# Performance work log

Measured on AMD Instinct MI355X. Metric: run time of the kernel, lower is better.

The kernel has to match this reference:

```python
import jax, jax.numpy as jnp
import numpy as np

B, T, N, DIN, U, K, C = 32, 256, 128, 16, 64, 2, 4
M = K + 1  # num diffusion matrices per support (I, P, 2P^2-I, ...)


def setup_inputs() -> dict:
    key = jax.random.key(0)
    ks = jax.random.split(key, 10)
    w = lambda k, shape: jax.random.normal(k, shape, jnp.float32) * 0.05
    inp = {}
    inp["input_seq"] = jax.random.normal(ks[0], (B, T, N, DIN), jnp.float32)
    inp["seq_lengths"] = jax.random.randint(ks[1], (B,), 1, T + 1)
    # scaled dense support (graph laplacian surrogate) for numerical stability
    inp["support"] = jax.random.normal(ks[2], (N, N), jnp.float32) / N
    inp["W0_gate"] = w(ks[3], ((DIN + U) * M, 2 * U))
    inp["b0_gate"] = jnp.ones((2 * U,), jnp.float32)  # bias_start=1.0
    inp["W0_cand"] = w(ks[4], ((DIN + U) * M, U))
    inp["b0_cand"] = jnp.zeros((U,), jnp.float32)
    inp["W1_gate"] = w(ks[5], (2 * U * M, 2 * U))
    inp["b1_gate"] = jnp.ones((2 * U,), jnp.float32)
    inp["W1_cand"] = w(ks[6], (2 * U * M, U))
    inp["b1_cand"] = jnp.zeros((U,), jnp.float32)
    inp["W_fc"] = w(ks[7], (U, C))
    inp["b_fc"] = jnp.zeros((C,), jnp.float32)
    return inp


def _gconv(x, support, W, b):
    # x: (B, N, Cin). Chebyshev-style diffusion: [x, Px, 2P(Px)-x, ...]
    x0 = x
    x1 = jnp.einsum('mn,bnc->bmc', support, x0)
    xs = [x0, x1]
    for _ in range(2, K + 1):
        x2 = 2.0 * jnp.einsum('mn,bnc->bmc', support, x1) - x0
        xs.append(x2)
        x0, x1 = x1, x2
    # stack on last axis -> (B, N, Cin, M) -> (B, N, Cin*M), matching the
    # torch reshape order (input feature major, matrix minor)
    xc = jnp.stack(xs, axis=-1).reshape(x.shape[0], x.shape[1], -1)
    return xc @ W + b


def _cell(x, h, support, Wg, bg, Wc, bc):
    # x: (B,N,Din), h: (B,N,U)
    val = jax.nn.sigmoid(_gconv(jnp.concatenate([x, h], axis=-1), support, Wg, bg))
    r, u = jnp.split(val, 2, axis=-1)
    c = jnp.tanh(_gconv(jnp.concatenate([x, r * h], axis=-1), support, Wc, bc))
    return u * h + (1.0 - u) * c


def _run_layer(x_seq, support, Wg, bg, Wc, bc):
    # x_seq: (T, B, N, D)
    def step(h, x):
        h2 = _cell(x, h, support, Wg, bg, Wc, bc)
        return h2, h2
    h0 = jnp.zeros((x_seq.shape[1], N, U), x_seq.dtype)
    _, out = jax.lax.scan(step, h0, x_seq)
    return out  # (T, B, N, U)


def reference(input_seq, seq_lengths, support, W0_gate, b0_gate, W0_cand, b0_cand,
              W1_gate, b1_gate, W1_cand, b1_cand, W_fc, b_fc):
    x = jnp.transpose(input_seq, (1, 0, 2, 3))  # (T,B,N,DIN)
    h1 = _run_layer(x, support, W0_gate, b0_gate, W0_cand, b0_cand)
    h2 = _run_layer(h1, support, W1_gate, b1_gate, W1_cand, b1_cand)
    out_seq = jnp.transpose(h2, (1, 0, 2, 3))  # (B,T,N,U)
    idx = seq_lengths - 1  # last relevant timestep per sequence
    last = out_seq[jnp.arange(out_seq.shape[0]), idx]  # (B,N,U)
    # dropout is identity in eval mode
    logits = jax.nn.relu(last) @ W_fc + b_fc  # (B,N,C)
    return jnp.max(logits, axis=1)  # max-pool over nodes -> (B,C)
```

## Files before the change

kernel.cpp:

```cpp
#include <hip/hip_runtime.h>

#define B_   32
#define T_   256
#define N_   128
#define DIN_ 16
#define U_   64

#define PD 456
#define PT 136
#define LDS_BYTES ((N_*PD + N_*PT)*2)

#define WT0G_OFF 0
#define WT0C_OFF (128*256)
#define WT1G_OFF (WT0C_OFF + 64*256)
#define WT1C_OFF (WT1G_OFF + 128*384)
#define WT_TOTAL (WT1C_OFF + 64*384)
#define S2_OFF   WT_TOTAL
#define FIFO_OFF (S2_OFF + 128*128)
#define FIFO_SLOT(bb,tt) (FIFO_OFF + ((bb)*8 + ((tt)&7))*8192)
#define FLG_BYTE ((FIFO_OFF + 32*8*8192)*2)
#define FLG_USH  4096
#define FIFO2_OFF (FIFO_OFF + 32*8*8192 + FLG_USH)
#define FIFO2_SLOT(bb,tt) (FIFO2_OFF + ((bb)*4 + ((tt)&3))*16384)

typedef __attribute__((ext_vector_type(8))) short bfrag;
typedef __attribute__((ext_vector_type(4))) float ffrag;
typedef __attribute__((ext_vector_type(4))) unsigned short us4;
typedef __attribute__((ext_vector_type(2))) unsigned short us2;
typedef unsigned long long ull;

#define SYNC() asm volatile("s_waitcnt lgkmcnt(0)\n\ts_barrier" ::: "memory")
#define MFMA16(a,b,c) __builtin_amdgcn_mfma_f32_16x16x32_bf16(a,b,c,0,0,0)

__device__ __forceinline__ unsigned short f2b(float x) {
  union { float f; unsigned u; } v; v.f = x;
  return (unsigned short)((v.u + 0x7fffu + ((v.u >> 16) & 1u)) >> 16);
}
__device__ __forceinline__ float sigm(float x) {
  float e = __expf(-x);
  return __builtin_amdgcn_rcpf(1.f + e);
}
__device__ __forceinline__ float tanh_(float x) {
  float e = __expf(2.f * x);
  return 1.f - 2.f * __builtin_amdgcn_rcpf(1.f + e);
}

__device__ __forceinline__ float wval0(const float* w, int ncol, int co, int k) {
  if (k < 16)  return w[(k*3+0)*ncol+co] - w[(k*3+2)*ncol+co];
  if (k < 48)  { int j=k-16, c=j>>1;
                 return (j&1) ? 2.f*w[(c*3+2)*ncol+co] : w[(c*3+1)*ncol+co]; }
  if (k < 64)  return 0.f;
  if (k < 128) { int c=16+(k-64); return w[(c*3+0)*ncol+co] - w[(c*3+2)*ncol+co]; }
  { int j=k-128, c=16+(j>>1);
    return (j&1) ? 2.f*w[(c*3+2)*ncol+co] : w[(c*3+1)*ncol+co]; }
}
__device__ __forceinline__ float wval1(const float* w, int ncol, int co, int k) {
  if (k < 64)  return w[(k*3+0)*ncol+co] - w[(k*3+2)*ncol+co];
  if (k < 192) { int j=k-64, c=j>>1;
                 return (j&1) ? 2.f*w[(c*3+2)*ncol+co] : w[(c*3+1)*ncol+co]; }
  if (k < 256) { int c=64+(k-192); return w[(c*3+0)*ncol+co] - w[(c*3+2)*ncol+co]; }
  { int j=k-256, c=64+(j>>1);
    return (j&1) ? 2.f*w[(c*3+2)*ncol+co] : w[(c*3+1)*ncol+co]; }
}
__device__ __forceinline__ float wval0c(const float* w, int ncol, int co, int k) {
  if (k < 64)  return wval0(w, ncol, co, k);
  if (k < 192) return wval0(w, ncol, co, k + 64);
  return wval0(w, ncol, co, k - 128);
}
__device__ __forceinline__ float wval1c(const float* w, int ncol, int co, int k) {
  if (k < 192) return wval1(w, ncol, co, k);
  if (k < 320) return wval1(w, ncol, co, k + 64);
  return wval1(w, ncol, co, k - 128);
}

__global__ void setup_wt(const float* __restrict__ w0g, const float* __restrict__ w0c,
                         const float* __restrict__ w1g, const float* __restrict__ w1c,
                         unsigned short* __restrict__ wt) {
  int i = blockIdx.x * blockDim.x + threadIdx.x;
  if (i >= WT_TOTAL) return;
  float v;
  if (i < WT0C_OFF)      { int co = i >> 8, k = i & 255;                 v = wval0 (w0g, 128, co, k); }
  else if (i < WT1G_OFF) { int j = i - WT0C_OFF; v = wval0c(w0c, 64, j >> 8, j & 255); }
  else if (i < WT1C_OFF) { int j = i - WT1G_OFF; v = wval1 (w1g, 128, j / 384, j % 384); }
  else                   { int j = i - WT1C_OFF; v = wval1c(w1c, 64, j / 384, j % 384); }
  wt[i] = f2b(v);
}

__global__ void setup_s2(const float* __restrict__ sup, unsigned short* __restrict__ s2) {
  int idx = blockIdx.x * blockDim.x + threadIdx.x;
  int i = idx >> 7, j = idx & 127;
  float acc = 0.f;
#pragma unroll 4
  for (int k = 0; k < 128; ++k) acc += sup[i*128 + k] * sup[k*128 + j];
  s2[idx] = f2b(acc);
}

__global__ void zero_flags(unsigned short* __restrict__ wt) {
  int* flg = (int*)((char*)wt + FLG_BYTE);
  for (int i = threadIdx.x; i < 2048; i += blockDim.x) flg[i] = 0;
}

template<int KT>
__device__ __forceinline__ void gateR(ffrag (&acc)[4][2],
    const bfrag (&bwr)[KT], const bfrag (&bwu)[KT],
    const unsigned short* __restrict__ arowB, const int lq) {
#pragma unroll
  for (int ks = 0; ks < KT; ++ks) {
    bfrag a[4];
#pragma unroll
    for (int i = 0; i < 4; ++i)
      a[i] = *(const bfrag*)&arowB[16*i*PD + 32*ks + 8*lq];
#pragma unroll
    for (int i = 0; i < 4; ++i) {
      acc[i][0] = MFMA16(a[i], bwr[ks], acc[i][0]);
      acc[i][1] = MFMA16(a[i], bwu[ks], acc[i][1]);
    }
  }
}
template<int KT>
__device__ __forceinline__ void candR(ffrag (&acc)[4], bfrag (&bw)[4],
    const unsigned short* __restrict__ arowB, const int (&kofs)[KT],
    const unsigned short* __restrict__ bpc, const int lq) {
#pragma unroll
  for (int ks = 0; ks < KT; ++ks) {
    const int k = ks & 3;
    bfrag a[4];
#pragma unroll
    for (int i = 0; i < 4; ++i)
      a[i] = *(const bfrag*)&arowB[16*i*PD + kofs[ks] + 8*lq];
    bfrag bc = bw[k];
    if (ks + 4 < KT) bw[k] = *(const bfrag*)&bpc[32*(ks+4) + 8*lq];
#pragma unroll
    for (int i = 0; i < 4; ++i) acc[i] = MFMA16(a[i], bc, acc[i]);
  }
}

__global__ __launch_bounds__(512, 2) void dcgru(
    const float* __restrict__ xseq, const int* __restrict__ slen,
    const float* __restrict__ sup,
    const float* __restrict__ b0g, const float* __restrict__ b0c,
    const float* __restrict__ b1g, const float* __restrict__ b1c,
    const float* __restrict__ wfc, const float* __restrict__ bfc,
    unsigned short* __restrict__ wt, float* __restrict__ out) {
  extern __shared__ unsigned short lds[];
  unsigned short* diffb = lds;
  unsigned short* difT  = lds + N_*PD;
  const int b    = (blockIdx.x & 7) | ((blockIdx.x >> 4) << 3);
  const int eta  = (blockIdx.x >> 3) & 1;
  const int tid  = threadIdx.x;
  const int w    = tid >> 6;
  const int j    = w & 3;
  const int g    = w >> 2;
  const int ln   = tid & 15;
  const int lq   = (tid >> 4) & 3;
  const int L    = slen[b];
  int* flg  = (int*)((char*)wt + FLG_BYTE);
  int* prod = flg + b*32;
  int* cons = flg + 1024 + b*32;
  const unsigned short* __restrict__ arowB = diffb + (64*g + ln)*PD;
  const ffrag fz = {0.f, 0.f, 0.f, 0.f};

  bfrag Sf[4], S2f[4];
#pragma unroll
  for (int ks = 0; ks < 4; ++ks) {
    const float* pS = sup + (16*w + ln)*N_ + 32*ks + 8*lq;
    union { bfrag v; unsigned short u[8]; } tmp;
#pragma unroll
    for (int jj = 0; jj < 8; ++jj) tmp.u[jj] = f2b(pS[jj]);
    Sf[ks] = tmp.v;
    S2f[ks] = *(const bfrag*)&wt[S2_OFF + (16*w + ln)*N_ + 32*ks + 8*lq];
  }

  auto diffuse = [&](int nt, int colc) {
    bfrag bf[4];
#pragma unroll
    for (int ks = 0; ks < 4; ++ks)
      bf[ks] = *(const bfrag*)&difT[(16*nt + ln)*PT + 32*ks + 8*lq];
    ffrag a1 = fz, a2 = fz;
#pragma unroll
    for (int ks = 0; ks < 4; ++ks) {
      a1 = MFMA16(Sf[ks],  bf[ks], a1);
      a2 = MFMA16(S2f[ks], bf[ks], a2);
    }
    const int n0 = 16*w + 4*lq;
    const int col = colc + 2*ln;
#pragma unroll
    for (int r = 0; r < 4; ++r) {
      us2 pq = {f2b(a1[r]), f2b(a2[r])};
      *(us2*)&diffb[(n0 + r)*PD + col] = pq;
    }
  };
  auto dumpCell = [&](ffrag (&v)[4], int colBase, int rowBase) {
    const int chh = 16*j + ln;
#pragma unroll
    for (int i = 0; i < 4; ++i) {
      const int n0 = 64*g + 16*i + 4*lq;
      unsigned short sv[4];
#pragma unroll
      for (int r = 0; r < 4; ++r) sv[r] = f2b(v[i][r]);
#pragma unroll
      for (int r = 0; r < 4; ++r) diffb[(n0 + r)*PD + colBase + chh] = sv[r];
      us4 q = {sv[0], sv[1], sv[2], sv[3]};
      *(us4*)&difT[(rowBase + chh)*PT + n0] = q;
    }
  };
  auto prebC = [&](bfrag (&bw)[4], const unsigned short* bpc) {
#pragma unroll
    for (int k = 0; k < 4; ++k) bw[k] = *(const bfrag*)&bpc[32*k + 8*lq];
  };
  auto waitge = [&](int* p, int seq) {
    if ((tid & 63) == 0) {
      int it = 0;
      while (__hip_atomic_load(p, __ATOMIC_RELAXED, __HIP_MEMORY_SCOPE_AGENT) < seq) {
        __builtin_amdgcn_s_sleep(1);
        if (++it > (1 << 24)) break;
      }
    }
  };

  bfrag bw4[4];

  if (eta == 0) {
    bfrag bwr[8], bwu[8];
    {
      const unsigned short* bpr = wt + WT0G_OFF + (16*j      + ln)*256;
      const unsigned short* bpu = wt + WT0G_OFF + (16*(4+j)  + ln)*256;
#pragma unroll
      for (int ks = 0; ks < 8; ++ks) {
        bwr[ks] = *(const bfrag*)&bpr[32*ks + 8*lq];
        bwu[ks] = *(const bfrag*)&bpu[32*ks + 8*lq];
      }
    }
    const unsigned short* bpc = wt + WT0C_OFF + (16*j + ln)*256;
    const float bgr = b0g[16*j + ln], bgu = b0g[64 + 16*j + ln];
    const float bcv = b0c[16*j + ln];
    const int kofs0[8] = {0, 32, 128, 160, 192, 224, 256, 288};
    ffrag h0m[4] = {fz, fz, fz, fz};

    for (int i = tid; i < N_*208; i += 512) {
      int row = i / 208, c = i - row*208;
      diffb[row*PD + 48 + c] = 0;
    }
    float4 xv = *(const float4*)&xseq[(size_t)(b*T_)*N_*DIN_ + 4*tid];

#pragma clang loop unroll(disable)
    for (int t = 0; t < L; ++t) {
      {
        const int node = tid >> 2, c = 4*(tid & 3);
        unsigned short s0 = f2b(xv.x), s1 = f2b(xv.y), s2 = f2b(xv.z), s3 = f2b(xv.w);
        us4 q = {s0, s1, s2, s3};
        *(us4*)&diffb[node*PD + c] = q;
        difT[(c+0)*PT + node] = s0; difT[(c+1)*PT + node] = s1;
        difT[(c+2)*PT + node] = s2; difT[(c+3)*PT + node] = s3;
        int tn = t + 1 < L ? t + 1 : L - 1;
        xv = *(const float4*)&xseq[(size_t)(b*T_ + tn)*N_*DIN_ + 4*tid];
      }
      SYNC();
      diffuse(0, 16);
      SYNC();
      ffrag u0s[4], rh[4];
      {
        ffrag ga[4][2] = {{fz, fz}, {fz, fz}, {fz, fz}, {fz, fz}};
        gateR<8>(ga, bwr, bwu, arowB, lq);
#pragma unroll
      for (int i = 0; i < 4; ++i)
#pragma unroll
          for (int r = 0; r < 4; ++r) {
            float rr = sigm(ga[i][0][r] + bgr);
            rh[i][r]  = rr * h0m[i][r];
            u0s[i][r] = sigm(ga[i][1][r] + bgu);
          }
      }
      dumpCell(rh, 256, 16);
      prebC(bw4, bpc);
      SYNC();
      diffuse(1, 128); diffuse(2, 160); diffuse(3, 192); diffuse(4, 224);
      SYNC();
      {
        ffrag ca[4] = {fz, fz, fz, fz};
        candR<8>(ca, bw4, arowB, kofs0, bpc, lq);
#pragma unroll
        for (int i = 0; i < 4; ++i)
#pragma unroll
          for (int r = 0; r < 4; ++r) {
            float cc = tanh_(ca[i][r] + bcv);
            float uu = u0s[i][r];
            h0m[i][r] = uu*h0m[i][r] + (1.f - uu)*cc;
          }
      }
      dumpCell(h0m, 64, 16);
      if (t >= 4) waitge(cons, t - 3);
      {
        unsigned short* slot = wt + FIFO_SLOT(b, t);
        const int chh = 16*j + ln;
#pragma unroll
        for (int i = 0; i < 4; ++i) {
          const int n0 = 64*g + 16*i + 4*lq;
          us4 q = {f2b(h0m[i][0]), f2b(h0m[i][1]), f2b(h0m[i][2]), f2b(h0m[i][3])};
          *(us4*)&slot[chh*128 + n0] = q;
        }
      }
      SYNC();
      diffuse(1, 128); diffuse(2, 160); diffuse(3, 192); diffuse(4, 224);
      SYNC();
      {
        unsigned short* slot2 = wt + FIFO2_SLOT(b, t);
#pragma unroll
        for (int rep = 0; rep < 8; ++rep) {
          const int i = tid + 512*rep;
          const int node = i >> 5, off = (i & 31)*4;
          ull v = *(const ull*)&diffb[node*PD + 128 + off];
          *(ull*)&slot2[node*128 + off] = v;
        }
      }
      asm volatile("s_waitcnt vmcnt(0)" ::: "memory");
      if ((tid & 63) == 0)
        __hip_atomic_fetch_add(prod, 1, __ATOMIC_RELEASE, __HIP_MEMORY_SCOPE_AGENT);
    }
    return;
  }

  {
    bfrag bwr[12], bwu[12];
    {
      const unsigned short* bpr = wt + WT1G_OFF + (16*j     + ln)*384;
      const unsigned short* bpu = wt + WT1G_OFF + (16*(4+j) + ln)*384;
#pragma unroll
      for (int ks = 0; ks < 12; ++ks) {
        bwr[ks] = *(const bfrag*)&bpr[32*ks + 8*lq];
        bwu[ks] = *(const bfrag*)&bpu[32*ks + 8*lq];
      }
    }
    const unsigned short* bpc = wt + WT1C_OFF + (16*j + ln)*384;
    const float bgr = b1g[16*j + ln], bgu = b1g[64 + 16*j + ln];
    const float bcv = b1c[16*j + ln];
    const int kofs1[12] = {0, 32, 64, 96, 128, 160, 256, 288, 320, 352, 384, 416};
    ffrag h1m[4] = {fz, fz, fz, fz};

#pragma clang loop unroll(disable)
    for (int t = 0; t < L; ++t) {
      waitge(prod, t + 1);
      {
        const unsigned short* slot = wt + FIFO_SLOT(b, t);
#pragma unroll
        for (int rep = 0; rep < 4; ++rep) {
          const int idx = tid + 512*rep;
          const int ch = idx >> 5, n0 = (idx & 31)*4;
          ull v = __hip_atomic_load((const ull*)&slot[ch*128 + n0],
                                    __ATOMIC_RELAXED, __HIP_MEMORY_SCOPE_AGENT);
          *(ull*)&difT[ch*PT + n0] = v;
          union { ull u; unsigned short s[4]; } cv; cv.u = v;
#pragma unroll
          for (int jj = 0; jj < 4; ++jj) diffb[(n0 + jj)*PD + ch] = cv.s[jj];
        }
        const unsigned short* slot2 = wt + FIFO2_SLOT(b, t);
#pragma unroll
        for (int rep = 0; rep < 8; ++rep) {
          const int i = tid + 512*rep;
          const int node = i >> 5, off = (i & 31)*4;
          ull v = __hip_atomic_load((const ull*)&slot2[node*128 + off],
                                    __ATOMIC_RELAXED, __HIP_MEMORY_SCOPE_AGENT);
          *(ull*)&diffb[node*PD + 64 + off] = v;
        }
        dumpCell(h1m, 192, 64);
      }
      SYNC();
      if (tid == 0)
        __hip_atomic_fetch_add(cons, 1, __ATOMIC_RELEASE, __HIP_MEMORY_SCOPE_AGENT);
      diffuse(4, 256); diffuse(5, 288); diffuse(6, 320); diffuse(7, 352);
      SYNC();
      ffrag u1s[4], rh[4];
      {
        ffrag ga[4][2] = {{fz, fz}, {fz, fz}, {fz, fz}, {fz, fz}};
        gateR<12>(ga, bwr, bwu, arowB, lq);
#pragma unroll
        for (int i = 0; i < 4; ++i)
#pragma unroll
          for (int r = 0; r < 4; ++r) {
            float rr = sigm(ga[i][0][r] + bgr);
            rh[i][r]  = rr * h1m[i][r];
            u1s[i][r] = sigm(ga[i][1][r] + bgu);
          }
      }
      dumpCell(rh, 384, 64);
      prebC(bw4, bpc);
      SYNC();
      diffuse(4, 256); diffuse(5, 288); diffuse(6, 320); diffuse(7, 352);
      SYNC();
      {
        ffrag ca[4] = {fz, fz, fz, fz};
        candR<12>(ca, bw4, arowB, kofs1, bpc, lq);
#pragma unroll
        for (int i = 0; i < 4; ++i)
#pragma unroll
          for (int r = 0; r < 4; ++r) {
            float cc = tanh_(ca[i][r] + bcv);
            float uu = u1s[i][r];
            h1m[i][r] = uu*h1m[i][r] + (1.f - uu)*cc;
          }
      }
      SYNC();
    }

    {
      float* hb = (float*)lds;
#pragma unroll
      for (int i = 0; i < 4; ++i)
#pragma unroll
        for (int r = 0; r < 4; ++r) {
          float v = h1m[i][r];
          hb[(64*g + 16*i + 4*lq + r)*U_ + 16*j + ln] = v > 0.f ? v : 0.f;
        }
    }
    __syncthreads();
    float* hb = (float*)lds;
    float* lb = hb + N_*U_;
    if (tid < N_) {
      float lg[4];
#pragma unroll
      for (int jj = 0; jj < 4; ++jj) lg[jj] = bfc[jj];
      for (int ch = 0; ch < U_; ++ch) {
        float v = hb[tid*U_ + ch];
#pragma unroll
        for (int jj = 0; jj < 4; ++jj) lg[jj] += v * wfc[ch*4 + jj];
      }
#pragma unroll
      for (int jj = 0; jj < 4; ++jj) lb[tid*4 + jj] = lg[jj];
    }
    __syncthreads();
    if (tid < 4) {
      float m = lb[tid];
      for (int n = 1; n < N_; ++n) m = fmaxf(m, lb[n*4 + tid]);
      out[b*4 + tid] = m;
    }
  }
}

extern "C" void kernel_launch(void* const* d_in, const int* in_sizes, int n_in,
                              void* d_out, int out_size, void* d_ws, size_t ws_size,
                              hipStream_t stream) {
  const float* xseq = (const float*)d_in[0];
  const int*   slen = (const int*)  d_in[1];
  const float* sup  = (const float*)d_in[2];
  const float* w0g  = (const float*)d_in[3];
  const float* b0g  = (const float*)d_in[4];
  const float* w0c  = (const float*)d_in[5];
  const float* b0c  = (const float*)d_in[6];
  const float* w1g  = (const float*)d_in[7];
  const float* b1g  = (const float*)d_in[8];
  const float* w1c  = (const float*)d_in[9];
  const float* b1c  = (const float*)d_in[10];
  const float* wfc  = (const float*)d_in[11];
  const float* bfc  = (const float*)d_in[12];
  float* out = (float*)d_out;
  unsigned short* wt = (unsigned short*)d_ws;

  (void)hipFuncSetAttribute((const void*)dcgru,
                            hipFuncAttributeMaxDynamicSharedMemorySize, LDS_BYTES);
  zero_flags<<<dim3(1), dim3(512), 0, stream>>>(wt);
  setup_wt<<<dim3((WT_TOTAL + 255)/256), dim3(256), 0, stream>>>(w0g, w0c, w1g, w1c, wt);
  setup_s2<<<dim3(64), dim3(256), 0, stream>>>(sup, wt + S2_OFF);
  dcgru<<<dim3(64), dim3(512), LDS_BYTES, stream>>>(
      xseq, slen, sup, b0g, b0c, b1g, b1c, wfc, bfc, wt, out);
}
```

Measured before the change: 2.533 ms.

## Double workgroup to 1024 threads, split node tiles and diffusion across wave halves

Doubles each block from 8 to 16 waves, so every wave now handles 32 nodes instead of 64 in the gate and candidate GEMMs. Diffusion tiles are split between the two wave halves. Gate weights are now streamed from global memory through a rolling 4-deep register buffer instead of being held fully in registers, which frees registers for the higher occupancy. Also changes the producer-flag wait threshold to 16*(t+1) and adds zero-initialisation of layer-1 diffusion columns. The risks are more barrier cost per wave, repeated weight reloads every step, and a flag protocol that only works if the producer increments the counter in a matching way.

```diff
diff --git a/kernel.cpp b/kernel.cpp
--- a/kernel.cpp
+++ b/kernel.cpp
@@ -101,41 +101,48 @@
 }
 
 template<int KT>
-__device__ __forceinline__ void gateR(ffrag (&acc)[4][2],
-    const bfrag (&bwr)[KT], const bfrag (&bwu)[KT],
+__device__ __forceinline__ void gateS(ffrag (&acc)[2][2],
+    bfrag (&br)[4], bfrag (&bu)[4],
+    const unsigned short* __restrict__ bpr, const unsigned short* __restrict__ bpu,
     const unsigned short* __restrict__ arowB, const int lq) {
 #pragma unroll
   for (int ks = 0; ks < KT; ++ks) {
-    bfrag a[4];
-#pragma unroll
-    for (int i = 0; i < 4; ++i)
+    const int k = ks & 3;
+    bfrag a[2];
+#pragma unroll
+    for (int i = 0; i < 2; ++i)
       a[i] = *(const bfrag*)&arowB[16*i*PD + 32*ks + 8*lq];
-#pragma unroll
-    for (int i = 0; i < 4; ++i) {
-      acc[i][0] = MFMA16(a[i], bwr[ks], acc[i][0]);
-      acc[i][1] = MFMA16(a[i], bwu[ks], acc[i][1]);
+    bfrag rc = br[k], uc = bu[k];
+    if (ks + 4 < KT) {
+      br[k] = *(const bfrag*)&bpr[32*(ks+4) + 8*lq];
+      bu[k] = *(const bfrag*)&bpu[32*(ks+4) + 8*lq];
+    }
+#pragma unroll
+    for (int i = 0; i < 2; ++i) {
+      acc[i][0] = MFMA16(a[i], rc, acc[i][0]);
+      acc[i][1] = MFMA16(a[i], uc, acc[i][1]);
     }
   }
 }
 template<int KT>
-__device__ __forceinline__ void candR(ffrag (&acc)[4], bfrag (&bw)[4],
+__device__ __forceinline__ void candR(ffrag (&acc)[2], bfrag (&bw)[4],
     const unsigned short* __restrict__ arowB, const int (&kofs)[KT],
     const unsigned short* __restrict__ bpc, const int lq) {
 #pragma unroll
   for (int ks = 0; ks < KT; ++ks) {
     const int k = ks & 3;
-    bfrag a[4];
-#pragma unroll
-    for (int i = 0; i < 4; ++i)
+    bfrag a[2];
+#pragma unroll
+    for (int i = 0; i < 2; ++i)
       a[i] = *(const bfrag*)&arowB[16*i*PD + kofs[ks] + 8*lq];
     bfrag bc = bw[k];
     if (ks + 4 < KT) bw[k] = *(const bfrag*)&bpc[32*(ks+4) + 8*lq];
 #pragma unroll
-    for (int i = 0; i < 4; ++i) acc[i] = MFMA16(a[i], bc, acc[i]);
+    for (int i = 0; i < 2; ++i) acc[i] = MFMA16(a[i], bc, acc[i]);
   }
 }
 
-__global__ __launch_bounds__(512, 2) void dcgru(
+__global__ __launch_bounds__(1024, 4) void dcgru(
     const float* __restrict__ xseq, const int* __restrict__ slen,
     const float* __restrict__ sup,
     const float* __restrict__ b0g, const float* __restrict__ b0c,
@@ -150,25 +157,27 @@
   const int tid  = threadIdx.x;
   const int w    = tid >> 6;
   const int j    = w & 3;
-  const int g    = w >> 2;
+  const int gm   = w >> 2;
+  const int ws   = w & 7;
+  const int hf   = w >> 3;
   const int ln   = tid & 15;
   const int lq   = (tid >> 4) & 3;
   const int L    = slen[b];
   int* flg  = (int*)((char*)wt + FLG_BYTE);
   int* prod = flg + b*32;
   int* cons = flg + 1024 + b*32;
-  const unsigned short* __restrict__ arowB = diffb + (64*g + ln)*PD;
+  const unsigned short* __restrict__ arowB = diffb + (32*gm + ln)*PD;
   const ffrag fz = {0.f, 0.f, 0.f, 0.f};
 
   bfrag Sf[4], S2f[4];
 #pragma unroll
   for (int ks = 0; ks < 4; ++ks) {
-    const float* pS = sup + (16*w + ln)*N_ + 32*ks + 8*lq;
+    const float* pS = sup + (16*ws + ln)*N_ + 32*ks + 8*lq;
     union { bfrag v; unsigned short u[8]; } tmp;
 #pragma unroll
     for (int jj = 0; jj < 8; ++jj) tmp.u[jj] = f2b(pS[jj]);
     Sf[ks] = tmp.v;
-    S2f[ks] = *(const bfrag*)&wt[S2_OFF + (16*w + ln)*N_ + 32*ks + 8*lq];
+    S2f[ks] = *(const bfrag*)&wt[S2_OFF + (16*ws + ln)*N_ + 32*ks + 8*lq];
   }
 
   auto diffuse = [&](int nt, int colc) {
@@ -182,7 +191,7 @@
       a1 = MFMA16(Sf[ks],  bf[ks], a1);
       a2 = MFMA16(S2f[ks], bf[ks], a2);
     }
-    const int n0 = 16*w + 4*lq;
+    const int n0 = 16*ws + 4*lq;
     const int col = colc + 2*ln;
 #pragma unroll
     for (int r = 0; r < 4; ++r) {
@@ -190,11 +199,11 @@
       *(us2*)&diffb[(n0 + r)*PD + col] = pq;
     }
   };
-  auto dumpCell = [&](ffrag (&v)[4], int colBase, int rowBase) {
+  auto dumpCell = [&](ffrag (&v)[2], int colBase, int rowBase) {
     const int chh = 16*j + ln;
 #pragma unroll
-    for (int i = 0; i < 4; ++i) {
-      const int n0 = 64*g + 16*i + 4*lq;
+    for (int i = 0; i < 2; ++i) {
+      const int n0 = 32*gm + 16*i + 4*lq;
       unsigned short sv[4];
 #pragma unroll
       for (int r = 0; r < 4; ++r) sv[r] = f2b(v[i][r]);
@@ -204,9 +213,9 @@
       *(us4*)&difT[(rowBase + chh)*PT + n0] = q;
     }
   };
-  auto prebC = [&](bfrag (&bw)[4], const unsigned short* bpc) {
-#pragma unroll
-    for (int k = 0; k < 4; ++k) bw[k] = *(const bfrag*)&bpc[32*k + 8*lq];
+  auto preb4 = [&](bfrag (&bw)[4], const unsigned short* bp) {
+#pragma unroll
+    for (int k = 0; k < 4; ++k) bw[k] = *(const bfrag*)&bp[32*k + 8*lq];
   };
   auto waitge = [&](int* p, int seq) {
     if ((tid & 63) == 0) {
@@ -218,52 +227,44 @@
     }
   };
 
-  bfrag bw4[4];
+  bfrag bw4[4], brg[4], bug[4];
 
   if (eta == 0) {
-    bfrag bwr[8], bwu[8];
-    {
-      const unsigned short* bpr = wt + WT0G_OFF + (16*j      + ln)*256;
-      const unsigned short* bpu = wt + WT0G_OFF + (16*(4+j)  + ln)*256;
-#pragma unroll
-      for (int ks = 0; ks < 8; ++ks) {
-        bwr[ks] = *(const bfrag*)&bpr[32*ks + 8*lq];
-        bwu[ks] = *(const bfrag*)&bpu[32*ks + 8*lq];
-      }
-    }
+    const unsigned short* bpr = wt + WT0G_OFF + (16*j      + ln)*256;
+    const unsigned short* bpu = wt + WT0G_OFF + (16*(4+j)  + ln)*256;
     const unsigned short* bpc = wt + WT0C_OFF + (16*j + ln)*256;
     const float bgr = b0g[16*j + ln], bgu = b0g[64 + 16*j + ln];
     const float bcv = b0c[16*j + ln];
     const int kofs0[8] = {0, 32, 128, 160, 192, 224, 256, 288};
-    ffrag h0m[4] = {fz, fz, fz, fz};
-
-    for (int i = tid; i < N_*208; i += 512) {
+    ffrag h0m[2] = {fz, fz};
+
+    for (int i = tid; i < N_*208; i += 1024) {
       int row = i / 208, c = i - row*208;
       diffb[row*PD + 48 + c] = 0;
     }
-    float4 xv = *(const float4*)&xseq[(size_t)(b*T_)*N_*DIN_ + 4*tid];
+    float2 xv = *(const float2*)&xseq[(size_t)(b*T_)*N_*DIN_ + 2*tid];
 
 #pragma clang loop unroll(disable)
     for (int t = 0; t < L; ++t) {
       {
-        const int node = tid >> 2, c = 4*(tid & 3);
-        unsigned short s0 = f2b(xv.x), s1 = f2b(xv.y), s2 = f2b(xv.z), s3 = f2b(xv.w);
-        us4 q = {s0, s1, s2, s3};
-        *(us4*)&diffb[node*PD + c] = q;
+        const int node = tid >> 3, c = 2*(tid & 7);
+        unsigned short s0 = f2b(xv.x), s1 = f2b(xv.y);
+        us2 q = {s0, s1};
+        *(us2*)&diffb[node*PD + c] = q;
         difT[(c+0)*PT + node] = s0; difT[(c+1)*PT + node] = s1;
-        difT[(c+2)*PT + node] = s2; difT[(c+3)*PT + node] = s3;
         int tn = t + 1 < L ? t + 1 : L - 1;
-        xv = *(const float4*)&xseq[(size_t)(b*T_ + tn)*N_*DIN_ + 4*tid];
-      }
-      SYNC();
-      diffuse(0, 16);
-      SYNC();
-      ffrag u0s[4], rh[4];
-      {
-        ffrag ga[4][2] = {{fz, fz}, {fz, fz}, {fz, fz}, {fz, fz}};
-        gateR<8>(ga, bwr, bwu, arowB, lq);
-#pragma unroll
-      for (int i = 0; i < 4; ++i)
+        xv = *(const float2*)&xseq[(size_t)(b*T_ + tn)*N_*DIN_ + 2*tid];
+      }
+      SYNC();
+      preb4(brg, bpr); preb4(bug, bpu);
+      if (hf == 0) diffuse(0, 16);
+      SYNC();
+      ffrag u0s[2], rh[2];
+      {
+        ffrag ga[2][2] = {{fz, fz}, {fz, fz}};
+        gateS<8>(ga, brg, bug, bpr, bpu, arowB, lq);
+#pragma unroll
+        for (int i = 0; i < 2; ++i)
 #pragma unroll
           for (int r = 0; r < 4; ++r) {
             float rr = sigm(ga[i][0][r] + bgr);
@@ -272,15 +273,16 @@
           }
       }
       dumpCell(rh, 256, 16);
-      prebC(bw4, bpc);
-      SYNC();
-      diffuse(1, 128); diffuse(2, 160); diffuse(3, 192); diffuse(4, 224);
-      SYNC();
-      {
-        ffrag ca[4] = {fz, fz, fz, fz};
+      preb4(bw4, bpc);
+      SYNC();
+      if (hf == 0) { diffuse(1, 128); diffuse(3, 192); }
+      else         { diffuse(2, 160); diffuse(4, 224); }
+      SYNC();
+      {
+        ffrag ca[2] = {fz, fz};
         candR<8>(ca, bw4, arowB, kofs0, bpc, lq);
 #pragma unroll
-        for (int i = 0; i < 4; ++i)
+        for (int i = 0; i < 2; ++i)
 #pragma unroll
           for (int r = 0; r < 4; ++r) {
             float cc = tanh_(ca[i][r] + bcv);
@@ -294,20 +296,21 @@
         unsigned short* slot = wt + FIFO_SLOT(b, t);
         const int chh = 16*j + ln;
 #pragma unroll
-        for (int i = 0; i < 4; ++i) {
-          const int n0 = 64*g + 16*i + 4*lq;
+        for (int i = 0; i < 2; ++i) {
+          const int n0 = 32*gm + 16*i + 4*lq;
           us4 q = {f2b(h0m[i][0]), f2b(h0m[i][1]), f2b(h0m[i][2]), f2b(h0m[i][3])};
           *(us4*)&slot[chh*128 + n0] = q;
         }
       }
       SYNC();
-      diffuse(1, 128); diffuse(2, 160); diffuse(3, 192); diffuse(4, 224);
+      if (hf == 0) { diffuse(1, 128); diffuse(3, 192); }
+      else         { diffuse(2, 160); diffuse(4, 224); }
       SYNC();
       {
         unsigned short* slot2 = wt + FIFO2_SLOT(b, t);
 #pragma unroll
-        for (int rep = 0; rep < 8; ++rep) {
-          const int i = tid + 512*rep;
+        for (int rep = 0; rep < 4; ++rep) {
+          const int i = tid + 1024*rep;
           const int node = i >> 5, off = (i & 31)*4;
           ull v = *(const ull*)&diffb[node*PD + 128 + off];
           *(ull*)&slot2[node*128 + off] = v;
@@ -321,30 +324,27 @@
   }
 
   {
-    bfrag bwr[12], bwu[12];
-    {
-      const unsigned short* bpr = wt + WT1G_OFF + (16*j     + ln)*384;
-      const unsigned short* bpu = wt + WT1G_OFF + (16*(4+j) + ln)*384;
-#pragma unroll
-      for (int ks = 0; ks < 12; ++ks) {
-        bwr[ks] = *(const bfrag*)&bpr[32*ks + 8*lq];
-        bwu[ks] = *(const bfrag*)&bpu[32*ks + 8*lq];
-      }
-    }
+    const unsigned short* bpr = wt + WT1G_OFF + (16*j     + ln)*384;
+    const unsigned short* bpu = wt + WT1G_OFF + (16*(4+j) + ln)*384;
     const unsigned short* bpc = wt + WT1C_OFF + (16*j + ln)*384;
     const float bgr = b1g[16*j + ln], bgu = b1g[64 + 16*j + ln];
     const float bcv = b1c[16*j + ln];
     const int kofs1[12] = {0, 32, 64, 96, 128, 160, 256, 288, 320, 352, 384, 416};
-    ffrag h1m[4] = {fz, fz, fz, fz};
+    ffrag h1m[2] = {fz, fz};
+
+    for (int i = tid; i < N_*192; i += 1024) {
+      int row = i / 192, c = i - row*192;
+      diffb[row*PD + 192 + c] = 0;
+    }
 
 #pragma clang loop unroll(disable)
     for (int t = 0; t < L; ++t) {
-      waitge(prod, t + 1);
+      waitge(prod, 16*(t + 1));
       {
         const unsigned short* slot = wt + FIFO_SLOT(b, t);
 #pragma unroll
-        for (int rep = 0; rep < 4; ++rep) {
-          const int idx = tid + 512*rep;
+        for (int rep = 0; rep < 2; ++rep) {
+          const int idx = tid + 1024*rep;
           const int ch = idx >> 5, n0 = (idx & 31)*4;
           ull v = __hip_atomic_load((const ull*)&slot[ch*128 + n0],
                                     __ATOMIC_RELAXED, __HIP_MEMORY_SCOPE_AGENT);
@@ -355,8 +355,8 @@
         }
         const unsigned short* slot2 = wt + FIFO2_SLOT(b, t);
 #pragma unroll
-        for (int rep = 0; rep < 8; ++rep) {
-          const int i = tid + 512*rep;
+        for (int rep = 0; rep < 4; ++rep) {
+          const int i = tid + 1024*rep;
           const int node = i >> 5, off = (i & 31)*4;
           ull v = __hip_atomic_load((const ull*)&slot2[node*128 + off],
                                     __ATOMIC_RELAXED, __HIP_MEMORY_SCOPE_AGENT);
@@ -367,14 +367,16 @@
       SYNC();
       if (tid == 0)
         __hip_atomic_fetch_add(cons, 1, __ATOMIC_RELEASE, __HIP_MEMORY_SCOPE_AGENT);
-      diffuse(4, 256); diffuse(5, 288); diffuse(6, 320); diffuse(7, 352);
-      SYNC();
-      ffrag u1s[4], rh[4];
-      {
-        ffrag ga[4][2] = {{fz, fz}, {fz, fz}, {fz, fz}, {fz, fz}};
-        gateR<12>(ga, bwr, bwu, arowB, lq);
-#pragma unroll
-        for (int i = 0; i < 4; ++i)
+      preb4(brg, bpr); preb4(bug, bpu);
+      if (hf == 0) { diffuse(4, 256); diffuse(6, 320); }
+      else         { diffuse(5, 288); diffuse(7, 352); }
+      SYNC();
+      ffrag u1s[2], rh[2];
+      {
+        ffrag ga[2][2] = {{fz, fz}, {fz, fz}};
+        gateS<12>(ga, brg, bug, bpr, bpu, arowB, lq);
+#pragma unroll
+        for (int i = 0; i < 2; ++i)
 #pragma unroll
           for (int r = 0; r < 4; ++r) {
             float rr = sigm(ga[i][0][r] + bgr);
@@ -383,15 +385,16 @@
           }
       }
       dumpCell(rh, 384, 64);
-      prebC(bw4, bpc);
-      SYNC();
-      diffuse(4, 256); diffuse(5, 288); diffuse(6, 320); diffuse(7, 352);
-      SYNC();
-      {
-        ffrag ca[4] = {fz, fz, fz, fz};
+      preb4(bw4, bpc);
+      SYNC();
+      if (hf == 0) { diffuse(4, 256); diffuse(6, 320); }
+      else         { diffuse(5, 288); diffuse(7, 352); }
+      SYNC();
+      {
+        ffrag ca[2] = {fz, fz};
         candR<12>(ca, bw4, arowB, kofs1, bpc, lq);
 #pragma unroll
-        for (int i = 0; i < 4; ++i)
+        for (int i = 0; i < 2; ++i)
 #pragma unroll
           for (int r = 0; r < 4; ++r) {
             float cc = tanh_(ca[i][r] + bcv);
@@ -405,11 +408,11 @@
     {
       float* hb = (float*)lds;
 #pragma unroll
-      for (int i = 0; i < 4; ++i)
+      for (int i = 0; i < 2; ++i)
 #pragma unroll
         for (int r = 0; r < 4; ++r) {
           float v = h1m[i][r];
-          hb[(64*g + 16*i + 4*lq + r)*U_ + 16*j + ln] = v > 0.f ? v : 0.f;
+          hb[(32*gm + 16*i + 4*lq + r)*U_ + 16*j + ln] = v > 0.f ? v : 0.f;
         }
     }
     __syncthreads();
@@ -460,6 +463,6 @@
   zero_flags<<<dim3(1), dim3(512), 0, stream>>>(wt);
   setup_wt<<<dim3((WT_TOTAL + 255)/256), dim3(256), 0, stream>>>(w0g, w0c, w1g, w1c, wt);
   setup_s2<<<dim3(64), dim3(256), 0, stream>>>(sup, wt + S2_OFF);
-  dcgru<<<dim3(64), dim3(512), LDS_BYTES, stream>>>(
+  dcgru<<<dim3(64), dim3(1024), LDS_BYTES, stream>>>(
       xseq, slen, sup, b0g, b0c, b1g, b1c, wfc, bfc, wt, out);
 }
```

Result: slower. 5.657 ms (+123.4%).
